# Kernel tuning notes

Measured on AMD Instinct MI355X. Metric: run time of the kernel, lower is better.

The kernel has to match this reference:

```python
import jax, jax.numpy as jnp
import numpy as np

N_DIM = 256
MAX_LEN = 256


def sincos_embedding(max_len, d):
    # standard transformer sin/cos positional embedding: (max_len, d)
    pos = np.arange(max_len, dtype=np.float32)[:, None]
    i = np.arange(d // 2, dtype=np.float32)
    angle = pos / np.power(10000.0, (2.0 * i) / d)
    pe = np.zeros((max_len, d), dtype=np.float32)
    pe[:, 0::2] = np.sin(angle)
    pe[:, 1::2] = np.cos(angle)
    return jnp.asarray(pe)


def setup_inputs() -> dict:
    key = jax.random.key(0)
    ks = jax.random.split(key, 7)
    B, C, H, W = 64, N_DIM, 8, 32
    s = 1.0 / np.sqrt(N_DIM)
    return {
        "x": jax.random.normal(ks[0], (B, C, H, W), dtype=jnp.float32),
        "seq_len": 26,
        "wo_w": jax.random.normal(ks[1], (N_DIM, N_DIM), dtype=jnp.float32) * s,
        "wo_b": jax.random.normal(ks[2], (N_DIM,), dtype=jnp.float32) * s,
        "wv_w": jax.random.normal(ks[3], (N_DIM, N_DIM), dtype=jnp.float32) * s,
        "wv_b": jax.random.normal(ks[4], (N_DIM,), dtype=jnp.float32) * s,
        "we_w": jax.random.normal(ks[5], (1, N_DIM), dtype=jnp.float32) * s,
        "we_b": jax.random.normal(ks[6], (1,), dtype=jnp.float32) * s,
    }


def reference(x, seq_len, wo_w, wo_b, wv_w, wv_b, we_w, we_b):
    B, C, H, W = x.shape
    D = C
    xh = jnp.transpose(x, (0, 2, 3, 1))  # (B, H, W, D)
    pe = sincos_embedding(MAX_LEN, D)[:seq_len]  # (T, D)
    # reading-state projection: (T, D) -> broadcast over batch
    att_r = pe @ wo_w.T + wo_b  # (T, D)
    # visual-feature projection
    att_x = xh @ wv_w.T + wv_b  # (B, H, W, D)
    # broadcast additive attention: (B, T, H, W, D)
    att = jnp.tanh(att_x[:, None] + att_r[None, :, None, None, :])
    score = jnp.einsum('bthwd,d->bthw', att, we_w[0]) + we_b[0]
    score = score.reshape(B, seq_len, H * W)
    alpha = jax.nn.softmax(score, axis=2)  # (B, T, HW)
    v = att_x.reshape(B, H * W, D)  # values are the wv projection
    # torch does mean over HW of alpha*v -> sum(alpha*v)/HW
    out = jnp.einsum('bts,bsd->btd', alpha, v) / (H * W)
    return out
```

## Files before the change

### kernel.cpp

```cpp
#include <hip/hip_runtime.h>

#define DD 256
#define BB 64
#define SS 256
#define K2 2.8853900817779268f
#define LOG2E 1.4426950408889634f

#if __has_builtin(__builtin_amdgcn_exp2f)
#define EXP2(x) __builtin_amdgcn_exp2f(x)
#else
#define EXP2(x) exp2f(x)
#endif

typedef __attribute__((ext_vector_type(8))) short bf16x8;
typedef __attribute__((ext_vector_type(4))) float f32x4;

static __device__ __forceinline__ float fast_rcp(float x) {
  return __builtin_amdgcn_rcpf(x);
}

__global__ __launch_bounds__(256) void k_prep(
    const float* __restrict__ wv_w,
    const float* __restrict__ wo_w, const float* __restrict__ wo_b,
    unsigned short* __restrict__ whi, unsigned short* __restrict__ wlo,
    float* __restrict__ att_r, int T)
{
  const int tid = threadIdx.x;
  if (blockIdx.x < 8) {
    const int cc = blockIdx.x;
#pragma unroll
    for (int sl = 0; sl < 4; ++sl) {
      const int slot = sl * 256 + tid;
      const int dt16 = slot >> 6;
      const int kg   = (slot >> 4) & 3;
      const int dcol = slot & 15;
      const int d  = dt16 * 16 + dcol;
      const int c0 = cc * 32 + kg * 8;
      float4 a = *reinterpret_cast<const float4*>(wv_w + (size_t)d * DD + c0);
      float4 b4 = *reinterpret_cast<const float4*>(wv_w + (size_t)d * DD + c0 + 4);
      const float wf[8] = {a.x, a.y, a.z, a.w, b4.x, b4.y, b4.z, b4.w};
      unsigned hp[4], lp[4];
#pragma unroll
      for (int p = 0; p < 4; ++p) {
        float fa = wf[p * 2], fb = wf[p * 2 + 1];
        unsigned ua = __float_as_uint(fa), ub = __float_as_uint(fb);
        hp[p] = (ua >> 16) | (ub & 0xffff0000u);
        float la = fa - __uint_as_float(ua & 0xffff0000u);
        float lb = fb - __uint_as_float(ub & 0xffff0000u);
        lp[p] = (__float_as_uint(la) >> 16) | (__float_as_uint(lb) & 0xffff0000u);
      }
      const size_t base = ((size_t)cc * 1024 + slot) * 8;
      *reinterpret_cast<uint4*>(whi + base) = make_uint4(hp[0], hp[1], hp[2], hp[3]);
      *reinterpret_cast<uint4*>(wlo + base) = make_uint4(lp[0], lp[1], lp[2], lp[3]);
    }
    return;
  }
  const int t = blockIdx.x - 8;
  if (t >= T) return;
  __shared__ float pe[DD];
  {
    int i = tid >> 1;
    double r = pow(10000.0, -(double)(2*i) / 256.0);
    double ang = (double)t * r;
    pe[tid] = (float)((tid & 1) ? cos(ang) : sin(ang));
  }
  __syncthreads();
  const float4* wr = reinterpret_cast<const float4*>(wo_w + (size_t)tid * DD);
  const float4* pp = reinterpret_cast<const float4*>(pe);
  float acc = 0.f;
#pragma unroll 8
  for (int k = 0; k < 64; ++k) {
    float4 w4 = wr[k]; float4 p4 = pp[k];
    acc = fmaf(w4.x, p4.x, acc);
    acc = fmaf(w4.y, p4.y, acc);
    acc = fmaf(w4.z, p4.z, acc);
    acc = fmaf(w4.w, p4.w, acc);
  }
  att_r[(size_t)t*DD + tid] = acc + wo_b[tid];
}

__global__ __launch_bounds__(256) void k_attx(
    const float* __restrict__ x,
    const unsigned short* __restrict__ whi, const unsigned short* __restrict__ wlo,
    const float* __restrict__ wv_b, float* __restrict__ att_x)
{
  const int b   = blockIdx.z;
  const int dq  = blockIdx.y;
  const int s0  = blockIdx.x * 64;
  const int tid = threadIdx.x;
  const int lane = tid & 63;
  const int wid  = tid >> 6;
  const int g    = lane >> 4;
  const int scol = lane & 15;
  const float* xcol = x + (size_t)b * DD * SS + s0 + wid * 16 + scol;

  f32x4 acc[4];
#pragma unroll
  for (int dtl = 0; dtl < 4; ++dtl) acc[dtl] = (f32x4){0.f, 0.f, 0.f, 0.f};

#pragma unroll
  for (int cc = 0; cc < 8; ++cc) {
    union { bf16x8 v; unsigned short u[8]; } ah, al;
#pragma unroll
    for (int j = 0; j < 8; ++j) {
      float f = xcol[(size_t)(cc * 32 + g * 8 + j) * SS];
      unsigned u = __float_as_uint(f);
      ah.u[j] = (unsigned short)(u >> 16);
      float fl = f - __uint_as_float(u & 0xffff0000u);
      al.u[j] = (unsigned short)(__float_as_uint(fl) >> 16);
    }
#pragma unroll
    for (int dtl = 0; dtl < 4; ++dtl) {
      const size_t base = ((size_t)cc * 1024 + (size_t)(dq * 4 + dtl) * 64 + lane) * 8;
      bf16x8 bh = *reinterpret_cast<const bf16x8*>(whi + base);
      bf16x8 bl = *reinterpret_cast<const bf16x8*>(wlo + base);
      acc[dtl] = __builtin_amdgcn_mfma_f32_16x16x32_bf16(ah.v, bh, acc[dtl], 0, 0, 0);
      acc[dtl] = __builtin_amdgcn_mfma_f32_16x16x32_bf16(ah.v, bl, acc[dtl], 0, 0, 0);
      acc[dtl] = __builtin_amdgcn_mfma_f32_16x16x32_bf16(al.v, bh, acc[dtl], 0, 0, 0);
    }
  }

  const int dcol = lane & 15, rg = lane >> 4;
#pragma unroll
  for (int dtl = 0; dtl < 4; ++dtl) {
    const int d = dq * 64 + dtl * 16 + dcol;
    float bv = wv_b[d];
#pragma unroll
    for (int r = 0; r < 4; ++r) {
      const int s = s0 + wid * 16 + rg * 4 + r;
      att_x[((size_t)(b * SS + s)) * DD + d] = acc[dtl][r] + bv;
    }
  }
}

__global__ __launch_bounds__(1024, 2) void k_score_out(
    const float* __restrict__ att_x, const float* __restrict__ att_r,
    const float* __restrict__ we_w, float* __restrict__ out, int T)
{
  const int b  = blockIdx.x;
  const int tq = blockIdx.y;
  const int tchunk = (T + 3) >> 2;
  const int t0 = tq * tchunk;
  const int nT = (T - t0 < tchunk) ? (T - t0) : tchunk;
  if (nT <= 0) return;
  const int tid = threadIdx.x;

  __shared__ float pool[4096];
  __shared__ float scS[8 * 256];
  __shared__ float mred[8][4];
  __shared__ float sred[8][4];

  for (int idx = tid; idx < nT * 256; idx += 1024) {
    int tl = idx >> 8, d = idx & 255;
    pool[tl * 320 + (d >> 4) * 20 + (d & 15)] = EXP2(att_r[(size_t)(t0 + tl) * DD + d] * K2);
  }
  for (int idx = tid; idx < 8 * 256; idx += 1024) scS[idx] = 0.f;

  const int sl = tid >> 4;
  const int c  = tid & 15;
  float4 w0, w1, w2, w3;
  {
    const float4* we4 = reinterpret_cast<const float4*>(we_w + c * 16);
    w0 = we4[0]; w1 = we4[1]; w2 = we4[2]; w3 = we4[3];
  }
  __syncthreads();

#pragma unroll
  for (int q = 0; q < 4; ++q) {
    const int s = q * 64 + sl;
    float f0x, f0y, f0z, f0w, f1x, f1y, f1z, f1w;
    float f2x, f2y, f2z, f2w, f3x, f3y, f3z, f3w;
    {
      const float4* ax4 = reinterpret_cast<const float4*>(
          att_x + ((size_t)(b * SS + s)) * DD + c * 16);
      float4 a = ax4[0], bq = ax4[1], cq = ax4[2], dq = ax4[3];
      f0x = EXP2(a.x*K2);  f0y = EXP2(a.y*K2);  f0z = EXP2(a.z*K2);  f0w = EXP2(a.w*K2);
      f1x = EXP2(bq.x*K2); f1y = EXP2(bq.y*K2); f1z = EXP2(bq.z*K2); f1w = EXP2(bq.w*K2);
      f2x = EXP2(cq.x*K2); f2y = EXP2(cq.y*K2); f2z = EXP2(cq.z*K2); f2w = EXP2(cq.w*K2);
      f3x = EXP2(dq.x*K2); f3y = EXP2(dq.y*K2); f3z = EXP2(dq.z*K2); f3w = EXP2(dq.w*K2);
    }
#pragma unroll 2
    for (int tl = 0; tl < nT; ++tl) {
      const float* aS = &pool[tl * 320 + c * 20];
      float4 a0 = *reinterpret_cast<const float4*>(aS);
      float4 a1 = *reinterpret_cast<const float4*>(aS + 4);
      float4 a2 = *reinterpret_cast<const float4*>(aS + 8);
      float4 a3 = *reinterpret_cast<const float4*>(aS + 12);
      float p0 = 0.f, p1 = 0.f, p2 = 0.f, p3 = 0.f;
      p0 = fmaf(w0.x, fast_rcp(fmaf(f0x, a0.x, 1.f)), p0);
      p0 = fmaf(w0.y, fast_rcp(fmaf(f0y, a0.y, 1.f)), p0);
      p0 = fmaf(w0.z, fast_rcp(fmaf(f0z, a0.z, 1.f)), p0);
      p0 = fmaf(w0.w, fast_rcp(fmaf(f0w, a0.w, 1.f)), p0);
      p1 = fmaf(w1.x, fast_rcp(fmaf(f1x, a1.x, 1.f)), p1);
      p1 = fmaf(w1.y, fast_rcp(fmaf(f1y, a1.y, 1.f)), p1);
      p1 = fmaf(w1.z, fast_rcp(fmaf(f1z, a1.z, 1.f)), p1);
      p1 = fmaf(w1.w, fast_rcp(fmaf(f1w, a1.w, 1.f)), p1);
      p2 = fmaf(w2.x, fast_rcp(fmaf(f2x, a2.x, 1.f)), p2);
      p2 = fmaf(w2.y, fast_rcp(fmaf(f2y, a2.y, 1.f)), p2);
      p2 = fmaf(w2.z, fast_rcp(fmaf(f2z, a2.z, 1.f)), p2);
      p2 = fmaf(w2.w, fast_rcp(fmaf(f2w, a2.w, 1.f)), p2);
      p3 = fmaf(w3.x, fast_rcp(fmaf(f3x, a3.x, 1.f)), p3);
      p3 = fmaf(w3.y, fast_rcp(fmaf(f3y, a3.y, 1.f)), p3);
      p3 = fmaf(w3.z, fast_rcp(fmaf(f3z, a3.z, 1.f)), p3);
      p3 = fmaf(w3.w, fast_rcp(fmaf(f3w, a3.w, 1.f)), p3);
      float part = (p0 + p1) + (p2 + p3);
      part += __shfl_xor(part, 1);
      part += __shfl_xor(part, 2);
      part += __shfl_xor(part, 4);
      part += __shfl_xor(part, 8);
      if (c == 0) scS[tl * 256 + s] = -2.f * part;
    }
  }
  __syncthreads();

  const int d   = tid & 255;
  const int scg = tid >> 8;
  const int wv4 = d >> 6;
#pragma unroll
  for (int pass = 0; pass < 2; ++pass) {
    const int r = pass * 4 + scg;
    const bool live = (r < nT);
    float v = live ? scS[r * 256 + d] : -3.0e38f;
    float m = v;
    m = fmaxf(m, __shfl_xor(m, 1));
    m = fmaxf(m, __shfl_xor(m, 2));
    m = fmaxf(m, __shfl_xor(m, 4));
    m = fmaxf(m, __shfl_xor(m, 8));
    m = fmaxf(m, __shfl_xor(m, 16));
    m = fmaxf(m, __shfl_xor(m, 32));
    if ((tid & 63) == 0) mred[r][wv4] = m;
    __syncthreads();
    float M = fmaxf(fmaxf(mred[r][0], mred[r][1]), fmaxf(mred[r][2], mred[r][3]));
    float ev = live ? EXP2((v - M) * LOG2E) : 0.f;
    float ss = ev;
    ss += __shfl_xor(ss, 1);
    ss += __shfl_xor(ss, 2);
    ss += __shfl_xor(ss, 4);
    ss += __shfl_xor(ss, 8);
    ss += __shfl_xor(ss, 16);
    ss += __shfl_xor(ss, 32);
    if ((tid & 63) == 0) sred[r][wv4] = ss;
    __syncthreads();
    float S = sred[r][0] + sred[r][1] + sred[r][2] + sred[r][3];
    if (live) scS[r * 256 + d] = ev * fast_rcp(S);
  }
  __syncthreads();

  float v[64];
  const float* ax = att_x + ((size_t)(b * SS) + scg * 64) * DD + d;
#pragma unroll
  for (int i = 0; i < 64; ++i) v[i] = ax[(size_t)i * DD];

#pragma unroll
  for (int half = 0; half < 2; ++half) {
    const int nR = (nT - half * 4 < 4) ? (nT - half * 4) : 4;
#pragma unroll
    for (int tl = 0; tl < 4; ++tl) {
      float a = 0.f;
#pragma unroll
      for (int i4 = 0; i4 < 16; ++i4) {
        float4 a4 = *reinterpret_cast<const float4*>(
            &scS[(half * 4 + tl) * 256 + scg * 64 + i4 * 4]);
        a = fmaf(a4.x, v[i4*4+0], a);
        a = fmaf(a4.y, v[i4*4+1], a);
        a = fmaf(a4.z, v[i4*4+2], a);
        a = fmaf(a4.w, v[i4*4+3], a);
      }
      pool[scg * 1024 + tl * 256 + d] = a;
    }
    __syncthreads();
    for (int idx = tid; idx < nR * 256; idx += 1024) {
      float sum = pool[idx] + pool[1024 + idx] + pool[2048 + idx] + pool[3072 + idx];
      out[((size_t)b * T + t0 + half * 4) * SS + idx] = sum * (1.0f / 256.0f);
    }
    __syncthreads();
  }
}

extern "C" void kernel_launch(void* const* d_in, const int* in_sizes, int n_in,
                              void* d_out, int out_size, void* d_ws, size_t ws_size,
                              hipStream_t stream) {
  (void)in_sizes; (void)n_in; (void)ws_size;
  const float* x    = (const float*)d_in[0];
  const float* wo_w = (const float*)d_in[2];
  const float* wo_b = (const float*)d_in[3];
  const float* wv_w = (const float*)d_in[4];
  const float* wv_b = (const float*)d_in[5];
  const float* we_w = (const float*)d_in[6];
  float* out = (float*)d_out;
  const int T = out_size / (BB * DD);

  float* att_x = (float*)d_ws;
  float* att_r = att_x + (size_t)BB * SS * DD;
  unsigned short* whi = (unsigned short*)(att_r + 32 * DD);
  unsigned short* wlo = whi + 65536;

  k_prep      <<<dim3(8 + T), 256, 0, stream>>>(wv_w, wo_w, wo_b, whi, wlo, att_r, T);
  k_attx      <<<dim3(4, 4, BB), 256, 0, stream>>>(x, whi, wlo, wv_b, att_x);
  k_score_out <<<dim3(BB, 4), 1024, 0, stream>>>(att_x, att_r, we_w, out, T);
}
```

Measured before the change: 57.76 us.

## Stage x and weight tiles in LDS with register prefetch in attx GEMM

The att_x projection kernel now loads x tiles and bf16 hi/lo weight tiles into shared memory with coalesced vector loads. It prefetches the next channel chunk into registers while the current one is computed. Each block covers 128 output columns instead of 64, so the grid is halved and each block reuses its x tile across twice as many MFMAs. The aim is to cut strided global x reads and redundant weight fetches, at the cost of more LDS, two barriers per chunk, and fewer blocks in flight.

```diff
diff --git a/kernel.cpp b/kernel.cpp
--- a/kernel.cpp
+++ b/kernel.cpp
@@ -85,50 +85,90 @@
     const float* __restrict__ wv_b, float* __restrict__ att_x)
 {
   const int b   = blockIdx.z;
-  const int dq  = blockIdx.y;
+  const int dT  = blockIdx.y;
   const int s0  = blockIdx.x * 64;
+  const int d0  = dT * 128;
   const int tid = threadIdx.x;
   const int lane = tid & 63;
   const int wid  = tid >> 6;
-  const int g    = lane >> 4;
-  const int scol = lane & 15;
-  const float* xcol = x + (size_t)b * DD * SS + s0 + wid * 16 + scol;
-
-  f32x4 acc[4];
-#pragma unroll
-  for (int dtl = 0; dtl < 4; ++dtl) acc[dtl] = (f32x4){0.f, 0.f, 0.f, 0.f};
-
-#pragma unroll
+  const float* xb = x + (size_t)b * DD * SS;
+  const uint4* whi4 = reinterpret_cast<const uint4*>(whi);
+  const uint4* wlo4 = reinterpret_cast<const uint4*>(wlo);
+
+  __shared__ float xls[32 * 65];
+  __shared__ uint4 wbh4[512];
+  __shared__ uint4 wbl4[512];
+
+  f32x4 acc[8];
+#pragma unroll
+  for (int dt = 0; dt < 8; ++dt) acc[dt] = (f32x4){0.f, 0.f, 0.f, 0.f};
+
+  const int cl = tid >> 3, sq = (tid & 7) * 8;
+  const float* xsrc = xb + (size_t)cl * SS + s0 + sq;
+  const int wofs = dT * 512;
+
+  uint4 wh0, wh1, wl0, wl1;
+  float4 xr0, xr1;
+  wh0 = whi4[wofs + tid];
+  wh1 = whi4[wofs + 256 + tid];
+  wl0 = wlo4[wofs + tid];
+  wl1 = wlo4[wofs + 256 + tid];
+  xr0 = *reinterpret_cast<const float4*>(xsrc);
+  xr1 = *reinterpret_cast<const float4*>(xsrc + 4);
+
   for (int cc = 0; cc < 8; ++cc) {
+    __syncthreads();
+    wbh4[tid]       = wh0;
+    wbh4[256 + tid] = wh1;
+    wbl4[tid]       = wl0;
+    wbl4[256 + tid] = wl1;
+    {
+      float* xd = &xls[cl * 65 + sq];
+      xd[0] = xr0.x; xd[1] = xr0.y; xd[2] = xr0.z; xd[3] = xr0.w;
+      xd[4] = xr1.x; xd[5] = xr1.y; xd[6] = xr1.z; xd[7] = xr1.w;
+    }
+    if (cc < 7) {
+      const int cb = (cc + 1) * 1024 + wofs;
+      wh0 = whi4[cb + tid];
+      wh1 = whi4[cb + 256 + tid];
+      wl0 = wlo4[cb + tid];
+      wl1 = wlo4[cb + 256 + tid];
+      const float* xn = xsrc + (size_t)(cc + 1) * 32 * SS;
+      xr0 = *reinterpret_cast<const float4*>(xn);
+      xr1 = *reinterpret_cast<const float4*>(xn + 4);
+    }
+    __syncthreads();
+    const int g = lane >> 4;
+    const int sA = wid * 16 + (lane & 15);
     union { bf16x8 v; unsigned short u[8]; } ah, al;
 #pragma unroll
     for (int j = 0; j < 8; ++j) {
-      float f = xcol[(size_t)(cc * 32 + g * 8 + j) * SS];
+      float f = xls[(g * 8 + j) * 65 + sA];
       unsigned u = __float_as_uint(f);
       ah.u[j] = (unsigned short)(u >> 16);
       float fl = f - __uint_as_float(u & 0xffff0000u);
       al.u[j] = (unsigned short)(__float_as_uint(fl) >> 16);
     }
 #pragma unroll
-    for (int dtl = 0; dtl < 4; ++dtl) {
-      const size_t base = ((size_t)cc * 1024 + (size_t)(dq * 4 + dtl) * 64 + lane) * 8;
-      bf16x8 bh = *reinterpret_cast<const bf16x8*>(whi + base);
-      bf16x8 bl = *reinterpret_cast<const bf16x8*>(wlo + base);
-      acc[dtl] = __builtin_amdgcn_mfma_f32_16x16x32_bf16(ah.v, bh, acc[dtl], 0, 0, 0);
-      acc[dtl] = __builtin_amdgcn_mfma_f32_16x16x32_bf16(ah.v, bl, acc[dtl], 0, 0, 0);
-      acc[dtl] = __builtin_amdgcn_mfma_f32_16x16x32_bf16(al.v, bh, acc[dtl], 0, 0, 0);
+    for (int dt = 0; dt < 8; ++dt) {
+      const int slot = (dt * 4 + g) * 16 + (lane & 15);
+      bf16x8 bh = *reinterpret_cast<const bf16x8*>(&wbh4[slot]);
+      bf16x8 bl = *reinterpret_cast<const bf16x8*>(&wbl4[slot]);
+      acc[dt] = __builtin_amdgcn_mfma_f32_16x16x32_bf16(ah.v, bh, acc[dt], 0, 0, 0);
+      acc[dt] = __builtin_amdgcn_mfma_f32_16x16x32_bf16(ah.v, bl, acc[dt], 0, 0, 0);
+      acc[dt] = __builtin_amdgcn_mfma_f32_16x16x32_bf16(al.v, bh, acc[dt], 0, 0, 0);
     }
   }
 
   const int dcol = lane & 15, rg = lane >> 4;
 #pragma unroll
-  for (int dtl = 0; dtl < 4; ++dtl) {
-    const int d = dq * 64 + dtl * 16 + dcol;
+  for (int dt = 0; dt < 8; ++dt) {
+    const int d = d0 + dt * 16 + dcol;
     float bv = wv_b[d];
 #pragma unroll
     for (int r = 0; r < 4; ++r) {
       const int s = s0 + wid * 16 + rg * 4 + r;
-      att_x[((size_t)(b * SS + s)) * DD + d] = acc[dtl][r] + bv;
+      att_x[((size_t)(b * SS + s)) * DD + d] = acc[dt][r] + bv;
     }
   }
 }
@@ -296,6 +336,6 @@
   unsigned short* wlo = whi + 65536;
 
   k_prep      <<<dim3(8 + T), 256, 0, stream>>>(wv_w, wo_w, wo_b, whi, wlo, att_r, T);
-  k_attx      <<<dim3(4, 4, BB), 256, 0, stream>>>(x, whi, wlo, wv_b, att_x);
+  k_attx      <<<dim3(4, 2, BB), 256, 0, stream>>>(x, whi, wlo, wv_b, att_x);
   k_score_out <<<dim3(BB, 4), 1024, 0, stream>>>(att_x, att_r, we_w, out, T);
 }
```

After: 55.44 us. -4.0%, faster.
